# Performance work log

Measured on AMD Instinct MI355X. Metric: run time of the kernel, lower is better.

The kernel has to match this reference:

```python
import jax, jax.numpy as jnp
import numpy as np

N = 4096          # in_features == out_features (mask [in,out] * weight [out,in] requires square)
TOKENS = 16384    # flattened (*, in_features) batch
WS_K = 4          # hardcoded in module __init__
WS_P = 0.5        # hardcoded in module __init__


def _ws_mask(n, k, p, seed=42):
    """Watts-Strogatz small-world adjacency mask, mirroring nx.watts_strogatz_graph.
    Ring lattice with k/2 neighbors each side, clockwise edges rewired with prob p."""
    rng = np.random.default_rng(seed)
    neigh = [set() for _ in range(n)]
    half = k // 2
    for j in range(1, half + 1):
        for i in range(n):
            t = (i + j) % n
            neigh[i].add(t)
            neigh[t].add(i)
    for j in range(1, half + 1):
        for i in range(n):
            t = (i + j) % n
            if rng.random() < p and t in neigh[i]:
                nt = int(rng.integers(n))
                tries = 0
                while (nt == i or nt in neigh[i]) and tries < 100:
                    nt = int(rng.integers(n))
                    tries += 1
                if nt != i and nt not in neigh[i]:
                    neigh[i].discard(t)
                    neigh[t].discard(i)
                    neigh[i].add(nt)
                    neigh[nt].add(i)
    mask = np.zeros((n, n), np.float32)
    for i in range(n):
        for t in neigh[i]:
            if t < n:  # neighbor < out_features guard (always true for square)
                mask[i, t] = 1.0
    return mask


def setup_inputs() -> dict:
    key = jax.random.key(0)
    k1, k2, k3 = jax.random.split(key, 3)
    x = jax.random.normal(k1, (TOKENS, N), dtype=jnp.float32)
    # kaiming_uniform_(a=sqrt(5)) on [out,in] -> U(-1/sqrt(in), 1/sqrt(in))
    bound = 1.0 / np.sqrt(N)
    weight = jax.random.uniform(k2, (N, N), minval=-bound, maxval=bound, dtype=jnp.float32)
    bias = jax.random.uniform(k3, (N,), minval=-bound, maxval=bound, dtype=jnp.float32)
    mask = jnp.asarray(_ws_mask(N, WS_K, WS_P))
    return {"x": x, "weight": weight, "bias": bias, "mask": mask}


def reference(x, weight, bias, mask):
    # y = x @ (W * M)^T + b   (F.linear with masked weight)
    w_masked = weight * mask                      # [out, in]
    return jnp.einsum("ti,oi->to", x, w_masked) + bias
```

## Files before the change

### kernel.cpp

```cpp
#include <hip/hip_runtime.h>

#define NN    4096
#define MAXD  32
#define WUNR  8
#define TB    4
#define BLK   512

__global__ __launch_bounds__(64) void build_ell_kernel(
    const float* __restrict__ weight, const float* __restrict__ mask,
    float2* __restrict__ ell, int* __restrict__ cnt) {
  const int o = blockIdx.x;
  const int lane = threadIdx.x;
  if (lane < MAXD) {
    float2 z; z.x = __uint_as_float(0u); z.y = 0.0f;
    ell[(size_t)lane * NN + o] = z;
  }
  __syncthreads();
  const float* mrow = mask + (size_t)o * NN;
  const float* wrow = weight + (size_t)o * NN;
  int count = 0;
  for (int base = 0; base < NN; base += 64) {
    const float m = mrow[base + lane];
    const bool nz = (m != 0.0f);
    const unsigned long long bal = __ballot(nz);
    if (nz) {
      const int pos = count + __popcll(bal & ((1ull << lane) - 1ull));
      if (pos < MAXD) {
        float2 e;
        e.x = __uint_as_float((unsigned)(base + lane));
        e.y = wrow[base + lane] * m;
        ell[(size_t)pos * NN + o] = e;
      }
    }
    count += __popcll(bal);
  }
  if (lane == 0) cnt[o] = (count < MAXD) ? count : MAXD;
}

__global__ __launch_bounds__(BLK) void ws_spmm_kernel(
    const float* __restrict__ x, const float* __restrict__ bias,
    const float2* __restrict__ ell, const int* __restrict__ cnt,
    float* __restrict__ out) {
  __shared__ float xs[TB * NN];
  const int tid = threadIdx.x;
  const size_t t0 = (size_t)blockIdx.x * TB;

  const float4* __restrict__ xg = (const float4*)(x + t0 * NN);
  float4* xsv = (float4*)xs;
#pragma unroll
  for (int i = 0; i < (TB * NN / 4) / BLK; ++i)
    xsv[tid + i * BLK] = xg[tid + i * BLK];
  __syncthreads();

  for (int ob = 0; ob < NN; ob += BLK) {
    const int o = ob + tid;
    const int c = cnt[o];

    float2 e[WUNR];
#pragma unroll
    for (int j = 0; j < WUNR; ++j)
      e[j] = ell[(size_t)j * NN + o];

    float acc0 = 0.f, acc1 = 0.f, acc2 = 0.f, acc3 = 0.f;
#pragma unroll
    for (int j = 0; j < WUNR; ++j) {
      const unsigned ix = __float_as_uint(e[j].x);
      const float w = e[j].y;
      acc0 = fmaf(xs[ix],          w, acc0);
      acc1 = fmaf(xs[NN + ix],     w, acc1);
      acc2 = fmaf(xs[2 * NN + ix], w, acc2);
      acc3 = fmaf(xs[3 * NN + ix], w, acc3);
    }
    for (int j = WUNR; j < c; ++j) {
      const float2 et = ell[(size_t)j * NN + o];
      const unsigned ix = __float_as_uint(et.x);
      const float w = et.y;
      acc0 = fmaf(xs[ix],          w, acc0);
      acc1 = fmaf(xs[NN + ix],     w, acc1);
      acc2 = fmaf(xs[2 * NN + ix], w, acc2);
      acc3 = fmaf(xs[3 * NN + ix], w, acc3);
    }

    const float b = bias[o];
    float* op = out + t0 * NN + o;
    op[0]      = acc0 + b;
    op[NN]     = acc1 + b;
    op[2 * NN] = acc2 + b;
    op[3 * NN] = acc3 + b;
  }
}

extern "C" void kernel_launch(void* const* d_in, const int* in_sizes, int n_in,
                              void* d_out, int out_size, void* d_ws, size_t ws_size,
                              hipStream_t stream) {
  const float* x      = (const float*)d_in[0];
  const float* weight = (const float*)d_in[1];
  const float* bias   = (const float*)d_in[2];
  const float* mask   = (const float*)d_in[3];
  float* out = (float*)d_out;

  char* ws = (char*)d_ws;
  float2* ell = (float2*)ws;
  int*    cnt = (int*)(ws + (size_t)MAXD * NN * sizeof(float2));

  const int tokens = in_sizes[0] / NN;

  build_ell_kernel<<<NN, 64, 0, stream>>>(weight, mask, ell, cnt);
  ws_spmm_kernel<<<tokens / TB, BLK, 0, stream>>>(x, bias, ell, cnt, out);
}
```

Before: 183.6 us.

## Interleave token tile in LDS as float4 and double block size

The shared-memory copy of the four-token x tile is transposed so each input column is stored as one float4. Each gathered neighbor then takes one 128-bit LDS read instead of four scalar reads. The global load becomes four scalar strided-row loads per element instead of float4 loads. Block size goes from 512 to 1024 threads and the output loop is unrolled, which can reduce occupancy and raise register pressure per block.

```diff
diff --git a/kernel.cpp b/kernel.cpp
--- a/kernel.cpp
+++ b/kernel.cpp
@@ -4,7 +4,7 @@
 #define MAXD  32
 #define WUNR  8
 #define TB    4
-#define BLK   512
+#define BLK   1024
 
 __global__ __launch_bounds__(64) void build_ell_kernel(
     const float* __restrict__ weight, const float* __restrict__ mask,
@@ -41,17 +41,24 @@
     const float* __restrict__ x, const float* __restrict__ bias,
     const float2* __restrict__ ell, const int* __restrict__ cnt,
     float* __restrict__ out) {
-  __shared__ float xs[TB * NN];
+  __shared__ float4 xs[NN];
   const int tid = threadIdx.x;
   const size_t t0 = (size_t)blockIdx.x * TB;
+  const float* __restrict__ xb = x + t0 * NN;
 
-  const float4* __restrict__ xg = (const float4*)(x + t0 * NN);
-  float4* xsv = (float4*)xs;
 #pragma unroll
-  for (int i = 0; i < (TB * NN / 4) / BLK; ++i)
-    xsv[tid + i * BLK] = xg[tid + i * BLK];
+  for (int i = 0; i < NN / BLK; ++i) {
+    const int c = tid + i * BLK;
+    float4 v;
+    v.x = xb[0 * NN + c];
+    v.y = xb[1 * NN + c];
+    v.z = xb[2 * NN + c];
+    v.w = xb[3 * NN + c];
+    xs[c] = v;
+  }
   __syncthreads();
 
+#pragma unroll
   for (int ob = 0; ob < NN; ob += BLK) {
     const int o = ob + tid;
     const int c = cnt[o];
@@ -66,19 +73,21 @@
     for (int j = 0; j < WUNR; ++j) {
       const unsigned ix = __float_as_uint(e[j].x);
       const float w = e[j].y;
-      acc0 = fmaf(xs[ix],          w, acc0);
-      acc1 = fmaf(xs[NN + ix],     w, acc1);
-      acc2 = fmaf(xs[2 * NN + ix], w, acc2);
-      acc3 = fmaf(xs[3 * NN + ix], w, acc3);
+      const float4 xv = xs[ix];
+      acc0 = fmaf(xv.x, w, acc0);
+      acc1 = fmaf(xv.y, w, acc1);
+      acc2 = fmaf(xv.z, w, acc2);
+      acc3 = fmaf(xv.w, w, acc3);
     }
     for (int j = WUNR; j < c; ++j) {
       const float2 et = ell[(size_t)j * NN + o];
       const unsigned ix = __float_as_uint(et.x);
       const float w = et.y;
-      acc0 = fmaf(xs[ix],          w, acc0);
-      acc1 = fmaf(xs[NN + ix],     w, acc1);
-      acc2 = fmaf(xs[2 * NN + ix], w, acc2);
-      acc3 = fmaf(xs[3 * NN + ix], w, acc3);
+      const float4 xv = xs[ix];
+      acc0 = fmaf(xv.x, w, acc0);
+      acc1 = fmaf(xv.y, w, acc1);
+      acc2 = fmaf(xv.z, w, acc2);
+      acc3 = fmaf(xv.w, w, acc3);
     }
 
     const float b = bias[o];
```

Result: no change. 185.0 us (+0.8%).

## Make SpMM blocks persistent with register-resident ELL and double-buffered token tiles

Applied to the files above, without the earlier changes.

Each block now handles 64 tokens over 16 rounds instead of 4 tokens. The ELL entries, counts and bias are loaded into registers once per block, so they are no longer reloaded for every 4-token group. Token tiles are stored interleaved as float4 so one LDS read returns all 4 tokens for a column, and the next round's tile is prefetched into registers and written to a second LDS buffer while the current one is computed. This cuts ELL traffic and hides x load latency, but raises register use at 1024 threads per block and reduces the grid to 256 blocks, which may lower occupancy.

```diff
diff --git a/kernel.cpp b/kernel.cpp
--- a/kernel.cpp
+++ b/kernel.cpp
@@ -1,10 +1,11 @@
 #include <hip/hip_runtime.h>
 
-#define NN    4096
-#define MAXD  32
-#define WUNR  8
-#define TB    4
-#define BLK   512
+#define NN     4096
+#define MAXD   32
+#define WUNR   8
+#define TB     4
+#define ROUNDS 16
+#define BLK    1024
 
 __global__ __launch_bounds__(64) void build_ell_kernel(
     const float* __restrict__ weight, const float* __restrict__ mask,
@@ -37,56 +38,98 @@
   if (lane == 0) cnt[o] = (count < MAXD) ? count : MAXD;
 }
 
-__global__ __launch_bounds__(BLK) void ws_spmm_kernel(
+__global__ __launch_bounds__(BLK, 4) void ws_spmm_kernel(
     const float* __restrict__ x, const float* __restrict__ bias,
     const float2* __restrict__ ell, const int* __restrict__ cnt,
     float* __restrict__ out) {
-  __shared__ float xs[TB * NN];
+  __shared__ float4 xs[2][NN];
   const int tid = threadIdx.x;
-  const size_t t0 = (size_t)blockIdx.x * TB;
+  const size_t tok0 = (size_t)blockIdx.x * (TB * ROUNDS);
 
-  const float4* __restrict__ xg = (const float4*)(x + t0 * NN);
-  float4* xsv = (float4*)xs;
+  float2 e[4][WUNR];
+  int   cn[4];
+  float bs[4];
 #pragma unroll
-  for (int i = 0; i < (TB * NN / 4) / BLK; ++i)
-    xsv[tid + i * BLK] = xg[tid + i * BLK];
+  for (int q = 0; q < 4; ++q) {
+    const int o = q * BLK + tid;
+    cn[q] = cnt[o];
+    bs[q] = bias[o];
+#pragma unroll
+    for (int j = 0; j < WUNR; ++j)
+      e[q][j] = ell[(size_t)j * NN + o];
+  }
+
+  {
+    const float* __restrict__ xb = x + tok0 * NN;
+#pragma unroll
+    for (int i = 0; i < NN / BLK; ++i) {
+      const int c2 = tid + i * BLK;
+      float4 v;
+      v.x = xb[0 * NN + c2];
+      v.y = xb[1 * NN + c2];
+      v.z = xb[2 * NN + c2];
+      v.w = xb[3 * NN + c2];
+      xs[0][c2] = v;
+    }
+  }
   __syncthreads();
 
-  for (int ob = 0; ob < NN; ob += BLK) {
-    const int o = ob + tid;
-    const int c = cnt[o];
+  for (int it = 0; it < ROUNDS; ++it) {
+    const int cur = it & 1;
 
-    float2 e[WUNR];
+    float xr[TB][NN / BLK];
+    if (it + 1 < ROUNDS) {
+      const float* __restrict__ xb = x + (tok0 + (size_t)(it + 1) * TB) * NN;
 #pragma unroll
-    for (int j = 0; j < WUNR; ++j)
-      e[j] = ell[(size_t)j * NN + o];
-
-    float acc0 = 0.f, acc1 = 0.f, acc2 = 0.f, acc3 = 0.f;
+      for (int i = 0; i < NN / BLK; ++i) {
+        const int c2 = tid + i * BLK;
 #pragma unroll
-    for (int j = 0; j < WUNR; ++j) {
-      const unsigned ix = __float_as_uint(e[j].x);
-      const float w = e[j].y;
-      acc0 = fmaf(xs[ix],          w, acc0);
-      acc1 = fmaf(xs[NN + ix],     w, acc1);
-      acc2 = fmaf(xs[2 * NN + ix], w, acc2);
-      acc3 = fmaf(xs[3 * NN + ix], w, acc3);
-    }
-    for (int j = WUNR; j < c; ++j) {
-      const float2 et = ell[(size_t)j * NN + o];
-      const unsigned ix = __float_as_uint(et.x);
-      const float w = et.y;
-      acc0 = fmaf(xs[ix],          w, acc0);
-      acc1 = fmaf(xs[NN + ix],     w, acc1);
-      acc2 = fmaf(xs[2 * NN + ix], w, acc2);
-      acc3 = fmaf(xs[3 * NN + ix], w, acc3);
+        for (int t = 0; t < TB; ++t)
+          xr[t][i] = xb[t * NN + c2];
+      }
     }
 
-    const float b = bias[o];
-    float* op = out + t0 * NN + o;
-    op[0]      = acc0 + b;
-    op[NN]     = acc1 + b;
-    op[2 * NN] = acc2 + b;
-    op[3 * NN] = acc3 + b;
+    const size_t t0 = tok0 + (size_t)it * TB;
+#pragma unroll
+    for (int q = 0; q < 4; ++q) {
+      const int o = q * BLK + tid;
+      float a0 = 0.f, a1 = 0.f, a2 = 0.f, a3 = 0.f;
+#pragma unroll
+      for (int j = 0; j < WUNR; ++j) {
+        const unsigned ix = __float_as_uint(e[q][j].x);
+        const float w = e[q][j].y;
+        const float4 xv = xs[cur][ix];
+        a0 = fmaf(xv.x, w, a0);
+        a1 = fmaf(xv.y, w, a1);
+        a2 = fmaf(xv.z, w, a2);
+        a3 = fmaf(xv.w, w, a3);
+      }
+      for (int j = WUNR; j < cn[q]; ++j) {
+        const float2 et = ell[(size_t)j * NN + o];
+        const unsigned ix = __float_as_uint(et.x);
+        const float w = et.y;
+        const float4 xv = xs[cur][ix];
+        a0 = fmaf(xv.x, w, a0);
+        a1 = fmaf(xv.y, w, a1);
+        a2 = fmaf(xv.z, w, a2);
+        a3 = fmaf(xv.w, w, a3);
+      }
+      float* op = out + t0 * NN + o;
+      op[0]      = a0 + bs[q];
+      op[NN]     = a1 + bs[q];
+      op[2 * NN] = a2 + bs[q];
+      op[3 * NN] = a3 + bs[q];
+    }
+
+    if (it + 1 < ROUNDS) {
+      const int nxt = cur ^ 1;
+#pragma unroll
+      for (int i = 0; i < NN / BLK; ++i) {
+        const int c2 = tid + i * BLK;
+        xs[nxt][c2] = make_float4(xr[0][i], xr[1][i], xr[2][i], xr[3][i]);
+      }
+    }
+    __syncthreads();
   }
 }
 
@@ -106,5 +149,5 @@
   const int tokens = in_sizes[0] / NN;
 
   build_ell_kernel<<<NN, 64, 0, stream>>>(weight, mask, ell, cnt);
-  ws_spmm_kernel<<<tokens / TB, BLK, 0, stream>>>(x, bias, ell, cnt, out);
+  ws_spmm_kernel<<<tokens / (TB * ROUNDS), BLK, 0, stream>>>(x, bias, ell, cnt, out);
 }
```

Result: slower. 318.8 us (+73.7%).
